# Optimization experiments

Hardware: AMD Instinct MI355X
Metric: run time of the kernel (lower is better)

Reference implementation:

```python
import jax, jax.numpy as jnp
import numpy as np

D = 1024          # n_embd
E = 8             # n_experts
FF = 4 * D        # ffn hidden
CAP = 2048        # expert_capacity
W_IMP = 0.01
W_LOAD = 0.01
LAMBDA_Z = 0.001
W_PEN = 0.01
B, S = 4, 2048
T = B * S


def setup_inputs() -> dict:
    key = jax.random.key(0)
    ks = jax.random.split(key, 8)
    x = jax.random.normal(ks[0], (B, S, D), dtype=jnp.float32)
    gate_w = jax.random.normal(ks[1], (E, D), dtype=jnp.float32) * 0.02   # Linear(D,E) weight
    w1 = jax.random.normal(ks[2], (E, D, FF), dtype=jnp.float32) * 0.02   # c_fc weight per expert
    b1 = jnp.zeros((E, FF), dtype=jnp.float32)
    w2 = jax.random.normal(ks[3], (E, FF, D), dtype=jnp.float32) * 0.02   # c_proj weight per expert
    b2 = jnp.zeros((E, D), dtype=jnp.float32)
    rnd = jax.random.uniform(ks[4], (T,), dtype=jnp.float32)              # torch.rand_like(g2)
    return {"x": x, "gate_w": gate_w, "w1": w1, "b1": b1, "w2": w2, "b2": b2, "rnd": rnd}


def _dispatch_ffn_combine(xf, e_ids, pos, wts, mask, w1, b1, w2, b2):
    """Capacity-buffered dispatch -> grouped FFN -> weighted combine for one routing slot.
    xf: [T,D]; e_ids: [T] int; pos: [T] position within expert; wts: [T] combine weight
    (already zeroed where masked); mask: [T] bool within-capacity (and stochastic) mask."""
    pc = jnp.clip(pos, 0, CAP - 1)
    buf = jnp.zeros((E, CAP, xf.shape[-1]), xf.dtype)
    # masked tokens contribute zeros; valid positions are unique per expert so add == set
    buf = buf.at[e_ids, pc].add(xf * mask[:, None].astype(xf.dtype))
    h = jax.nn.gelu(jnp.einsum('ecd,edf->ecf', buf, w1) + b1[:, None, :], approximate=True)
    out = jnp.einsum('ecf,efd->ecd', h, w2) + b2[:, None, :]          # [E,C,D]
    return out[e_ids, pc] * wts[:, None]                               # [T,D]


def _forward(x, gate_w, w1, b1, w2, b2, rnd):
    xf = x.reshape(-1, x.shape[-1])                                    # [T,D]
    logits = xf @ gate_w.T                                             # [T,E] (bias=False)

    # auxiliary losses
    p166 = jax.nn.softmax(logits / 1.66, axis=-1)
    penalty_a = jnp.mean(p166 * (1.0 - p166))
    pm = p166.mean(axis=0)
    penalty_b = 1.0 / E - jnp.mean(pm * (1.0 - pm))
    penalty = W_PEN * (penalty_a + penalty_b)
    z_loss = LAMBDA_Z * jnp.mean(jax.nn.logsumexp(logits, axis=-1) ** 2)

    probs = jax.nn.softmax(logits.astype(jnp.float32), axis=-1).astype(x.dtype)
    weights, sel = jax.lax.top_k(probs, 2)
    g1, g2 = weights[:, 0], weights[:, 1]
    e1, e2 = sel[:, 0], sel[:, 1]
    denom = g1 + g2
    g1n, g2n = g1 / denom, g2 / denom

    oh1 = jax.nn.one_hot(e1, E, dtype=jnp.int32)
    pos1 = jnp.take_along_axis(jnp.cumsum(oh1, axis=0), e1[:, None], axis=1)[:, 0] - 1
    mask1 = pos1 < CAP
    w_slot1 = g1n * mask1.astype(x.dtype)

    oh2 = jax.nn.one_hot(e2, E, dtype=jnp.int32)
    pos2 = jnp.take_along_axis(jnp.cumsum(oh2, axis=0), e2[:, None], axis=1)[:, 0] - 1
    mask2 = (pos2 < CAP) & (rnd < 2.0 * g2n)
    w_slot2 = g2n * mask2.astype(x.dtype)

    # load-balance loss: f_i from top-1 one-hot, P_i from softmax probs
    f_i = oh1.astype(jnp.float32).mean(axis=0)
    P_i = probs.mean(axis=0)
    load_loss = W_LOAD * E * jnp.sum(f_i * P_i)

    # importance loss over combine matrix G (column sums)
    imp = jnp.zeros((E,), x.dtype).at[e1].add(w_slot1).at[e2].add(w_slot2)
    mean = imp.mean()
    var = jnp.var(imp)
    imp_loss = W_IMP * var / (mean ** 2)

    aux = penalty + z_loss + load_loss + imp_loss

    y = _dispatch_ffn_combine(xf, e1, pos1, w_slot1, mask1, w1, b1, w2, b2)
    y = y + _dispatch_ffn_combine(xf, e2, pos2, w_slot2, mask2, w1, b1, w2, b2)
    return y.reshape(x.shape), aux


def reference(x, gate_w, w1, b1, w2, b2, rnd):
    return _forward(x, gate_w, w1, b1, w2, b2, rnd)
```

## Files before the change

kernel.cpp:

```cpp
#include <hip/hip_runtime.h>
#include <math.h>
#include <stdint.h>

#define DD 1024
#define EE 8
#define FF 4096
#define CAPV 2048
#define TT 8192
#define LIST_STRIDE 4096

typedef __bf16 bf16x8 __attribute__((ext_vector_type(8)));
typedef __bf16 bf16x4 __attribute__((ext_vector_type(4)));
typedef float floatx4 __attribute__((ext_vector_type(4)));
typedef float floatx16 __attribute__((ext_vector_type(16)));

typedef __attribute__((address_space(3))) unsigned int as3_uint;
typedef __attribute__((address_space(1))) const unsigned int as1_uint;

__device__ __forceinline__ void gl_lds16(const void* g, void* l) {
    __builtin_amdgcn_global_load_lds((as1_uint*)g, (as3_uint*)l, 16, 0, 0);
}

__device__ __forceinline__ unsigned short f2bf(float f) {
    union { float f; unsigned int u; } v; v.f = f;
    const unsigned int r = v.u + 0x7FFFu + ((v.u >> 16) & 1u);
    return (unsigned short)(r >> 16);
}

#define GATE_BLOCKS 256
#define T1_BLOCKS 16384
#define T2_BLOCKS 16384

__device__ __forceinline__ void transpose_body(
    const float* __restrict__ in, __bf16* __restrict__ out,
    int K, int N, int bk, int bn, int e, float (*tile)[65], int tid)
{
    const float* ine = in + (size_t)e * K * N;
    __bf16* oute = out + (size_t)e * K * N;
    #pragma unroll
    for (int p = 0; p < 8; ++p) {
        const int idx = p * 256 + tid;
        const int kl = idx >> 5, nl = idx & 31;
        tile[nl][kl] = ine[(size_t)(bk + kl) * N + bn + nl];
    }
    __syncthreads();
    #pragma unroll
    for (int p = 0; p < 4; ++p) {
        const int wdx = p * 256 + tid;
        const int nl = wdx >> 5, c = wdx & 31;
        const unsigned int pk = (unsigned int)f2bf(tile[nl][c * 2])
                              | ((unsigned int)f2bf(tile[nl][c * 2 + 1]) << 16);
        *(unsigned int*)&oute[(size_t)(bn + nl) * K + bk + c * 2] = pk;
    }
}

__global__ __launch_bounds__(256) void moe_prep_kernel(
    const float* __restrict__ x, const float* __restrict__ gw,
    int* __restrict__ e1o, int* __restrict__ e2o,
    float* __restrict__ g1o, float* __restrict__ g2o,
    float* __restrict__ sums, __bf16* __restrict__ xb,
    const float* __restrict__ w1, __bf16* __restrict__ w1T,
    const float* __restrict__ w2, __bf16* __restrict__ w2T)
{
    __shared__ float smem[EE * DD];
    __shared__ float wp[4][26];
    const int bid = blockIdx.x;
    const int tid = threadIdx.x;

    if (bid >= GATE_BLOCKS) {
        float (*tile)[65] = (float (*)[65])smem;
        if (bid < GATE_BLOCKS + T1_BLOCKS) {
            const int f = bid - GATE_BLOCKS;
            transpose_body(w1, w1T, DD, FF, (f & 15) * 64, ((f >> 4) & 127) * 32,
                           f >> 11, tile, tid);
        } else {
            const int f = bid - GATE_BLOCKS - T1_BLOCKS;
            transpose_body(w2, w2T, FF, DD, (f & 63) * 64, ((f >> 6) & 31) * 32,
                           f >> 11, tile, tid);
        }
        return;
    }

    float (*sgw)[DD] = (float (*)[DD])smem;
    for (int i = tid; i < EE * DD; i += 256) sgw[i >> 10][i & 1023] = gw[i];
    __syncthreads();

    const int wave = tid >> 6, lane = tid & 63;
    const int gwave = bid * 4 + wave;
    const int nwaves = GATE_BLOCKS * 4;

    float pa_acc = 0.f, z_acc = 0.f;
    float P_acc[EE] = {0}, p6_acc[EE] = {0};
    int n1_acc[EE] = {0};

    for (int t = gwave; t < TT; t += nwaves) {
        float acc[EE] = {0};
        const float* xr = x + (size_t)t * DD;
        __bf16* xbr = xb + (size_t)t * DD;
        #pragma unroll
        for (int i = 0; i < DD / 64; ++i) {
            const float xv = xr[lane + 64 * i];
            xbr[lane + 64 * i] = (__bf16)xv;
            #pragma unroll
            for (int e = 0; e < EE; ++e) acc[e] += xv * sgw[e][lane + 64 * i];
        }
        #pragma unroll
        for (int e = 0; e < EE; ++e) {
            float v = acc[e];
            #pragma unroll
            for (int off = 32; off > 0; off >>= 1) v += __shfl_xor(v, off, 64);
            acc[e] = v;
        }
        if (lane == 0) {
            float mx = acc[0];
            #pragma unroll
            for (int e = 1; e < EE; ++e) mx = fmaxf(mx, acc[e]);
            float pr[EE], p6[EE], se = 0.f, s6 = 0.f;
            #pragma unroll
            for (int e = 0; e < EE; ++e) {
                pr[e] = __expf(acc[e] - mx); se += pr[e];
                p6[e] = __expf((acc[e] - mx) * (1.0f / 1.66f)); s6 += p6[e];
            }
            const float lse = mx + __logf(se);
            z_acc += lse * lse;
            const float ise = 1.f / se, is6 = 1.f / s6;
            #pragma unroll
            for (int e = 0; e < EE; ++e) {
                pr[e] *= ise; p6[e] *= is6;
                P_acc[e] += pr[e]; p6_acc[e] += p6[e];
                pa_acc += p6[e] * (1.f - p6[e]);
            }
            int a = 0;
            #pragma unroll
            for (int e = 1; e < EE; ++e) if (pr[e] > pr[a]) a = e;
            int b = (a == 0) ? 1 : 0;
            #pragma unroll
            for (int e = 0; e < EE; ++e) if (e != a && pr[e] > pr[b]) b = e;
            n1_acc[a]++;
            const float ga = pr[a], gb = pr[b], idn = 1.f / (ga + gb);
            e1o[t] = a; e2o[t] = b;
            g1o[t] = ga * idn; g2o[t] = gb * idn;
        }
    }
    if (lane == 0) {
        wp[wave][0] = pa_acc; wp[wave][1] = z_acc;
        #pragma unroll
        for (int e = 0; e < EE; ++e) {
            wp[wave][2 + e] = P_acc[e]; wp[wave][10 + e] = p6_acc[e];
            wp[wave][18 + e] = (float)n1_acc[e];
        }
    }
    __syncthreads();
    if (tid < 26) {
        const float s = wp[0][tid] + wp[1][tid] + wp[2][tid] + wp[3][tid];
        atomicAdd(&sums[tid], s);
    }
}

__global__ __launch_bounds__(256) void moe_scan_kernel(
    const int* __restrict__ e1i, const int* __restrict__ e2i,
    const float* __restrict__ g1i, const float* __restrict__ g2i,
    const float* __restrict__ rnd, const float* __restrict__ sums,
    int* __restrict__ etok, int* __restrict__ p1o, int* __restrict__ p2o,
    int* __restrict__ cnt1, int* __restrict__ cnt2,
    float* __restrict__ imp1, float* __restrict__ imp2)
{
    const int bid = blockIdx.x, slot = bid >> 3, e = bid & 7;
    const int tid = threadIdx.x, wave = tid >> 6, lane = tid & 63;
    __shared__ int wtA[4], wtB[4];
    __shared__ float red[256];
    const int* ev = slot ? e2i : e1i;
    const float* gv = slot ? g2i : g1i;
    int* po = slot ? p2o : p1o;
    const int base = slot ? min((int)sums[18 + e], CAPV) : 0;

    int runTot = 0, runM = 0;
    float limp = 0.f;
    for (int c = 0; c < TT / 256; ++c) {
        const int t = c * 256 + tid;
        const int sel = (ev[t] == e) ? 1 : 0;
        const float w = gv[t];
        int ps = sel;
        #pragma unroll
        for (int off = 1; off < 64; off <<= 1) { int v = __shfl_up(ps, off, 64); if (lane >= off) ps += v; }
        if (lane == 63) wtA[wave] = ps;
        __syncthreads();
        int wpre = 0, ctot = 0;
        #pragma unroll
        for (int ww = 0; ww < 4; ++ww) { if (ww < wave) wpre += wtA[ww]; ctot += wtA[ww]; }
        const int pos = runTot + wpre + ps - 1;
        int m, idx;
        if (slot == 0) {
            m = sel && (pos < CAPV);
            idx = pos;
        } else {
            m = (sel && (pos < CAPV) && (rnd[t] < 2.f * w)) ? 1 : 0;
            int pm = m;
            #pragma unroll
            for (int off = 1; off < 64; off <<= 1) { int v = __shfl_up(pm, off, 64); if (lane >= off) pm += v; }
            if (lane == 63) wtB[wave] = pm;
            __syncthreads();
            int wpm = 0, mtot = 0;
            #pragma unroll
            for (int ww = 0; ww < 4; ++ww) { if (ww < wave) wpm += wtB[ww]; mtot += wtB[ww]; }
            idx = runM + wpm + pm - 1;
            runM += mtot;
        }
        if (sel) po[t] = m ? (e * LIST_STRIDE + base + idx) : -1;
        if (m) {
            etok[e * LIST_STRIDE + base + idx] = t;
            limp += w;
        }
        runTot += ctot;
        __syncthreads();
    }
    red[tid] = limp; __syncthreads();
    for (int s = 128; s > 0; s >>= 1) { if (tid < s) red[tid] += red[tid + s]; __syncthreads(); }
    if (tid == 0) {
        if (slot == 0) { cnt1[e] = min(runTot, CAPV); imp1[e] = red[0]; }
        else           { cnt2[e] = runM;              imp2[e] = red[0]; }
    }
}

__global__ void moe_aux_kernel(const float* __restrict__ sums,
                               const float* __restrict__ imp1, const float* __restrict__ imp2,
                               float* __restrict__ out_aux)
{
    if (threadIdx.x != 0 || blockIdx.x != 0) return;
    const float invT = 1.f / (float)TT;
    const float pa = sums[0] / ((float)TT * (float)EE);
    float pb = 0.f, load = 0.f, msum = 0.f;
    float im[EE];
    for (int e = 0; e < EE; ++e) {
        const float pm = sums[10 + e] * invT;
        pb += pm * (1.f - pm);
        load += (sums[18 + e] * invT) * (sums[2 + e] * invT);
        im[e] = imp1[e] + imp2[e];
        msum += im[e];
    }
    pb = 1.f / (float)EE - pb / (float)EE;
    const float penalty = 0.01f * (pa + pb);
    const float z_loss = 0.001f * sums[1] * invT;
    const float load_loss = 0.01f * (float)EE * load;
    const float mean = msum / (float)EE;
    float var = 0.f;
    for (int e = 0; e < EE; ++e) { const float d = im[e] - mean; var += d * d; }
    var /= (float)EE;
    const float imp_loss = 0.01f * var / (mean * mean);
    *out_aux = penalty + z_loss + load_loss + imp_loss;
}

#define FFN_CORE32(NT)                                                         \
    stage(0, 0);                                                               \
    stage(1, 64);                                                              \
    asm volatile("s_waitcnt vmcnt(8)" ::: "memory");                           \
    __builtin_amdgcn_s_barrier();                                              \
    for (int t = 0; t < (NT); ++t) {                                           \
        const int cur = t & 1;                                                 \
        _Pragma("unroll")                                                      \
        for (int ks = 0; ks < 4; ++ks) {                                       \
            bf16x8 av[4], bv[2];                                               \
            const int ch = ((ks * 2 + hi) ^ kx) * 8;                           \
            _Pragma("unroll")                                                  \
            for (int mi = 0; mi < 4; ++mi)                                     \
                av[mi] = *(const bf16x8*)&As[cur][ar[mi] + ch];                 \
            _Pragma("unroll")                                                  \
            for (int nj = 0; nj < 2; ++nj)                                     \
                bv[nj] = *(const bf16x8*)&Bs[cur][br[nj] + ch];                 \
            __builtin_amdgcn_s_setprio(1);                                     \
            _Pragma("unroll")                                                  \
            for (int mi = 0; mi < 4; ++mi)                                     \
                _Pragma("unroll")                                              \
                for (int nj = 0; nj < 2; ++nj)                                 \
                    acc[mi][nj] = __builtin_amdgcn_mfma_f32_32x32x16_bf16(     \
                        bv[nj], av[mi], acc[mi][nj], 0, 0, 0);                 \
            __builtin_amdgcn_s_setprio(0);                                     \
        }                                                                      \
        asm volatile("s_waitcnt lgkmcnt(0)" ::: "memory");                     \
        __builtin_amdgcn_s_barrier();                                          \
        if (t < (NT) - 2) {                                                    \
            stage(cur, (t + 2) * 64);                                          \
            asm volatile("s_waitcnt vmcnt(8)" ::: "memory");                   \
        } else {                                                               \
            asm volatile("s_waitcnt vmcnt(0)" ::: "memory");                   \
        }                                                                      \
        __builtin_amdgcn_s_barrier();                                          \
    }

__global__ __launch_bounds__(512, 2) void moe_ffn1_mfma(
    const __bf16* __restrict__ xb, const __bf16* __restrict__ w1T,
    const float* __restrict__ b1, const int* __restrict__ etok,
    const int* __restrict__ cnt1, const int* __restrict__ cnt2,
    __bf16* __restrict__ H)
{
    const int f = blockIdx.x;
    const int xcd = f & 7, s = f >> 3;
    const int g = xcd * 16 + (s >> 4);
    const int e = g >> 4, n0 = (g & 15) * 256;
    const int m0 = (s & 15) * 256;
    const int ce = cnt1[e] + cnt2[e];
    if (m0 >= ce) return;
    const int tid = threadIdx.x, lane = tid & 63, w = tid >> 6;
    const int wm = w >> 2, wn = w & 3;
    const int l32 = lane & 31, hi = lane >> 5;
    const int kx = l32 & 7;

    __shared__ __bf16 As[2][16384];
    __shared__ __bf16 Bs[2][16384];

    const int srow = tid >> 3;
    const int srcoff = ((tid & 7) ^ (srow & 7)) * 8;
    const __bf16* ap[4];
    const __bf16* bp[4];
    const __bf16* bbase = w1T + (size_t)e * FF * DD;
    #pragma unroll
    for (int r = 0; r < 4; ++r) {
        const int gr = m0 + r * 64 + srow;
        const int tok = (gr < ce) ? etok[e * LIST_STRIDE + gr] : 0;
        ap[r] = xb + (size_t)tok * DD + srcoff;
        bp[r] = bbase + (size_t)(n0 + r * 64 + srow) * DD + srcoff;
    }
    const int ldst = w * 512;

    floatx16 acc[4][2];
    #pragma unroll
    for (int i = 0; i < 4; ++i)
        #pragma unroll
        for (int j = 0; j < 2; ++j)
            #pragma unroll
            for (int q = 0; q < 16; ++q) acc[i][j][q] = 0.f;

    int ar[4], br[2];
    #pragma unroll
    for (int mi = 0; mi < 4; ++mi) ar[mi] = (wm * 128 + mi * 32 + l32) * 64;
    #pragma unroll
    for (int nj = 0; nj < 2; ++nj) br[nj] = (wn * 64 + nj * 32 + l32) * 64;

    auto stage = [&](int bufi, int koff) {
        #pragma unroll
        for (int r = 0; r < 4; ++r)
            gl_lds16(ap[r] + koff, &As[bufi][r * 4096 + ldst]);
        #pragma unroll
        for (int r = 0; r < 4; ++r)
            gl_lds16(bp[r] + koff, &Bs[bufi][r * 4096 + ldst]);
    };

    FFN_CORE32(16)

    const float* b1e = b1 + (size_t)e * FF;
    #pragma unroll
    for (int mi = 0; mi < 4; ++mi) {
        const int mrow = m0 + wm * 128 + mi * 32 + l32;
        __bf16* hrow = H + ((size_t)e * LIST_STRIDE + mrow) * FF;
        #pragma unroll
        for (int nj = 0; nj < 2; ++nj)
            #pragma unroll
            for (int rg = 0; rg < 4; ++rg) {
                const int col0 = n0 + wn * 64 + nj * 32 + rg * 8 + hi * 4;
                const float4 bb = *(const float4*)&b1e[col0];
                float vv[4] = {acc[mi][nj][rg * 4 + 0] + bb.x,
                               acc[mi][nj][rg * 4 + 1] + bb.y,
                               acc[mi][nj][rg * 4 + 2] + bb.z,
                               acc[mi][nj][rg * 4 + 3] + bb.w};
                bf16x4 pk;
                #pragma unroll
                for (int r = 0; r < 4; ++r) {
                    const float v = vv[r];
                    const float u = 0.7978845608028654f * (v + 0.044715f * v * v * v);
                    const float th = 1.f - 2.f / (__expf(2.f * u) + 1.f);
                    pk[r] = (__bf16)(0.5f * v * (1.f + th));
                }
                *(bf16x4*)&hrow[col0] = pk;
            }
    }
}

__global__ __launch_bounds__(512, 2) void moe_ffn2_mfma(
    const __bf16* __restrict__ H, const __bf16* __restrict__ w2T,
    const float* __restrict__ b2, const int* __restrict__ cnt1,
    const int* __restrict__ cnt2, __bf16* __restrict__ O)
{
    const int f = blockIdx.x;
    const int xcd = f & 7, s = f >> 3;
    const int g = xcd * 4 + (s >> 4);
    const int e = g >> 2, n0 = (g & 3) * 256;
    const int m0 = (s & 15) * 256;
    const int ce = cnt1[e] + cnt2[e];
    if (m0 >= ce) return;
    const int tid = threadIdx.x, lane = tid & 63, w = tid >> 6;
    const int wm = w >> 2, wn = w & 3;
    const int l32 = lane & 31, hi = lane >> 5;
    const int kx = l32 & 7;

    __shared__ __bf16 As[2][16384];
    __shared__ __bf16 Bs[2][16384];

    const int srow = tid >> 3;
    const int srcoff = ((tid & 7) ^ (srow & 7)) * 8;
    const __bf16* ap[4];
    const __bf16* bp[4];
    const __bf16* bbase = w2T + (size_t)e * DD * FF;
    #pragma unroll
    for (int r = 0; r < 4; ++r) {
        ap[r] = H + ((size_t)e * LIST_STRIDE + m0 + r * 64 + srow) * FF + srcoff;
        bp[r] = bbase + (size_t)(n0 + r * 64 + srow) * FF + srcoff;
    }
    const int ldst = w * 512;

    floatx16 acc[4][2];
    #pragma unroll
    for (int i = 0; i < 4; ++i)
        #pragma unroll
        for (int j = 0; j < 2; ++j)
            #pragma unroll
            for (int q = 0; q < 16; ++q) acc[i][j][q] = 0.f;

    int ar[4], br[2];
    #pragma unroll
    for (int mi = 0; mi < 4; ++mi) ar[mi] = (wm * 128 + mi * 32 + l32) * 64;
    #pragma unroll
    for (int nj = 0; nj < 2; ++nj) br[nj] = (wn * 64 + nj * 32 + l32) * 64;

    auto stage = [&](int bufi, int koff) {
        #pragma unroll
        for (int r = 0; r < 4; ++r)
            gl_lds16(ap[r] + koff, &As[bufi][r * 4096 + ldst]);
        #pragma unroll
        for (int r = 0; r < 4; ++r)
            gl_lds16(bp[r] + koff, &Bs[bufi][r * 4096 + ldst]);
    };

    FFN_CORE32(64)

    const float* b2e = b2 + (size_t)e * DD;
    #pragma unroll
    for (int mi = 0; mi < 4; ++mi) {
        const int grow = m0 + wm * 128 + mi * 32 + l32;
        if (grow < ce) {
            __bf16* orow = O + ((size_t)e * LIST_STRIDE + grow) * DD;
            #pragma unroll
            for (int nj = 0; nj < 2; ++nj)
                #pragma unroll
                for (int rg = 0; rg < 4; ++rg) {
                    const int col0 = n0 + wn * 64 + nj * 32 + rg * 8 + hi * 4;
                    const float4 bb = *(const float4*)&b2e[col0];
                    bf16x4 pk;
                    pk[0] = (__bf16)(acc[mi][nj][rg * 4 + 0] + bb.x);
                    pk[1] = (__bf16)(acc[mi][nj][rg * 4 + 1] + bb.y);
                    pk[2] = (__bf16)(acc[mi][nj][rg * 4 + 2] + bb.z);
                    pk[3] = (__bf16)(acc[mi][nj][rg * 4 + 3] + bb.w);
                    *(bf16x4*)&orow[col0] = pk;
                }
        }
    }
}

__global__ __launch_bounds__(256) void moe_combine_kernel(
    const __bf16* __restrict__ O, const float* __restrict__ g1v,
    const float* __restrict__ g2v, const int* __restrict__ p1v,
    const int* __restrict__ p2v, float* __restrict__ y)
{
    const int t = blockIdx.x;
    const int col = threadIdx.x * 4;
    const int p1 = p1v[t], p2 = p2v[t];
    float4 r = make_float4(0.f, 0.f, 0.f, 0.f);
    if (p1 >= 0) {
        const float g = g1v[t];
        const bf16x4 v = *(const bf16x4*)&O[(size_t)p1 * DD + col];
        r.x += g * (float)v[0]; r.y += g * (float)v[1];
        r.z += g * (float)v[2]; r.w += g * (float)v[3];
    }
    if (p2 >= 0) {
        const float g = g2v[t];
        const bf16x4 v = *(const bf16x4*)&O[(size_t)p2 * DD + col];
        r.x += g * (float)v[0]; r.y += g * (float)v[1];
        r.z += g * (float)v[2]; r.w += g * (float)v[3];
    }
    *(float4*)&y[(size_t)t * DD + col] = r;
}

extern "C" void kernel_launch(void* const* d_in, const int* in_sizes, int n_in,
                              void* d_out, int out_size, void* d_ws, size_t ws_size,
                              hipStream_t stream) {
    const float* x   = (const float*)d_in[0];
    const float* gw  = (const float*)d_in[1];
    const float* w1  = (const float*)d_in[2];
    const float* b1  = (const float*)d_in[3];
    const float* w2  = (const float*)d_in[4];
    const float* b2  = (const float*)d_in[5];
    const float* rnd = (const float*)d_in[6];
    float* out = (float*)d_out;

    char* p = (char*)d_ws;
    float* sums = (float*)p;
    float* imp1 = (float*)(p + 128);
    float* imp2 = (float*)(p + 160);
    int*   cnt1 = (int*)(p + 192);
    int*   cnt2 = (int*)(p + 224);
    p += 512;
    int*   e1v = (int*)p;   p += TT * 4;
    int*   e2v = (int*)p;   p += TT * 4;
    float* g1v = (float*)p; p += TT * 4;
    float* g2v = (float*)p; p += TT * 4;
    int*   p1v = (int*)p;   p += TT * 4;
    int*   p2v = (int*)p;   p += TT * 4;
    int*   etok = (int*)p;  p += EE * LIST_STRIDE * 4;
    uintptr_t q = (((uintptr_t)p) + 255) & ~(uintptr_t)255;
    __bf16* xb  = (__bf16*)q;  q += (size_t)TT * DD * 2;
    __bf16* w1T = (__bf16*)q;  q += (size_t)EE * FF * DD * 2;
    __bf16* w2T = (__bf16*)q;  q += (size_t)EE * DD * FF * 2;
    __bf16* H   = (__bf16*)q;  q += (size_t)EE * LIST_STRIDE * FF * 2;
    __bf16* O   = (__bf16*)q;

    hipMemsetAsync(sums, 0, 128, stream);

    moe_prep_kernel<<<GATE_BLOCKS + T1_BLOCKS + T2_BLOCKS, 256, 0, stream>>>(
        x, gw, e1v, e2v, g1v, g2v, sums, xb, w1, w1T, w2, w2T);
    moe_scan_kernel<<<16, 256, 0, stream>>>(e1v, e2v, g1v, g2v, rnd, sums,
                                            etok, p1v, p2v, cnt1, cnt2, imp1, imp2);
    moe_aux_kernel<<<1, 64, 0, stream>>>(sums, imp1, imp2, out + (size_t)TT * DD);

    moe_ffn1_mfma<<<2048, 512, 0, stream>>>(xb, w1T, b1, etok, cnt1, cnt2, H);
    moe_ffn2_mfma<<<512, 512, 0, stream>>>(H, w2T, b2, cnt1, cnt2, O);
    moe_combine_kernel<<<TT, 256, 0, stream>>>(O, g1v, g2v, p1v, p2v, out);
}
```

Baseline: 764.9 us.

## Shrink FFN GEMM tiles to 128x128 with 16x16x32 MFMA and 256 threads

```diff
diff --git a/kernel.cpp b/kernel.cpp
--- a/kernel.cpp
+++ b/kernel.cpp
@@ -12,7 +12,6 @@
 typedef __bf16 bf16x8 __attribute__((ext_vector_type(8)));
 typedef __bf16 bf16x4 __attribute__((ext_vector_type(4)));
 typedef float floatx4 __attribute__((ext_vector_type(4)));
-typedef float floatx16 __attribute__((ext_vector_type(16)));
 
 typedef __attribute__((address_space(3))) unsigned int as3_uint;
 typedef __attribute__((address_space(1))) const unsigned int as1_uint;
@@ -250,44 +249,45 @@
     *out_aux = penalty + z_loss + load_loss + imp_loss;
 }
 
-#define FFN_CORE32(NT)                                                         \
+#define FFN_CORE128(NT)                                                        \
     stage(0, 0);                                                               \
-    stage(1, 64);                                                              \
-    asm volatile("s_waitcnt vmcnt(8)" ::: "memory");                           \
+    asm volatile("s_waitcnt vmcnt(0)" ::: "memory");                           \
     __builtin_amdgcn_s_barrier();                                              \
+    _Pragma("unroll 2")                                                        \
     for (int t = 0; t < (NT); ++t) {                                           \
         const int cur = t & 1;                                                 \
+        if (t + 1 < (NT)) stage(cur ^ 1, (t + 1) * 64);                        \
+        bf16x8 a0[4], a1[4], b0[4], b1[4];                                     \
         _Pragma("unroll")                                                      \
-        for (int ks = 0; ks < 4; ++ks) {                                       \
-            bf16x8 av[4], bv[2];                                               \
-            const int ch = ((ks * 2 + hi) ^ kx) * 8;                           \
-            _Pragma("unroll")                                                  \
-            for (int mi = 0; mi < 4; ++mi)                                     \
-                av[mi] = *(const bf16x8*)&As[cur][ar[mi] + ch];                 \
-            _Pragma("unroll")                                                  \
-            for (int nj = 0; nj < 2; ++nj)                                     \
-                bv[nj] = *(const bf16x8*)&Bs[cur][br[nj] + ch];                 \
-            __builtin_amdgcn_s_setprio(1);                                     \
-            _Pragma("unroll")                                                  \
-            for (int mi = 0; mi < 4; ++mi)                                     \
-                _Pragma("unroll")                                              \
-                for (int nj = 0; nj < 2; ++nj)                                 \
-                    acc[mi][nj] = __builtin_amdgcn_mfma_f32_32x32x16_bf16(     \
-                        bv[nj], av[mi], acc[mi][nj], 0, 0, 0);                 \
-            __builtin_amdgcn_s_setprio(0);                                     \
+        for (int i = 0; i < 4; ++i) {                                          \
+            a0[i] = *(const bf16x8*)&As[cur][ar[i] + sw0];                     \
+            a1[i] = *(const bf16x8*)&As[cur][ar[i] + sw1];                     \
+        }                                                                      \
+        _Pragma("unroll")                                                      \
+        for (int j = 0; j < 4; ++j) {                                          \
+            b0[j] = *(const bf16x8*)&Bs[cur][br[j] + sw0];                     \
+            b1[j] = *(const bf16x8*)&Bs[cur][br[j] + sw1];                     \
         }                                                                      \
         asm volatile("s_waitcnt lgkmcnt(0)" ::: "memory");                     \
+        __builtin_amdgcn_s_setprio(1);                                         \
+        _Pragma("unroll")                                                      \
+        for (int i = 0; i < 4; ++i)                                            \
+            _Pragma("unroll")                                                  \
+            for (int j = 0; j < 4; ++j)                                        \
+                acc[i][j] = __builtin_amdgcn_mfma_f32_16x16x32_bf16(           \
+                    b0[j], a0[i], acc[i][j], 0, 0, 0);                         \
+        _Pragma("unroll")                                                      \
+        for (int i = 0; i < 4; ++i)                                            \
+            _Pragma("unroll")                                                  \
+            for (int j = 0; j < 4; ++j)                                        \
+                acc[i][j] = __builtin_amdgcn_mfma_f32_16x16x32_bf16(           \
+                    b1[j], a1[i], acc[i][j], 0, 0, 0);                         \
+        __builtin_amdgcn_s_setprio(0);                                         \
+        asm volatile("s_waitcnt vmcnt(0)" ::: "memory");                       \
         __builtin_amdgcn_s_barrier();                                          \
-        if (t < (NT) - 2) {                                                    \
-            stage(cur, (t + 2) * 64);                                          \
-            asm volatile("s_waitcnt vmcnt(8)" ::: "memory");                   \
-        } else {                                                               \
-            asm volatile("s_waitcnt vmcnt(0)" ::: "memory");                   \
-        }                                                                      \
-        __builtin_amdgcn_s_barrier();                                          \
-    }
-
-__global__ __launch_bounds__(512, 2) void moe_ffn1_mfma(
+    }
+
+__global__ __launch_bounds__(256, 2) void moe_ffn1_mfma(
     const __bf16* __restrict__ xb, const __bf16* __restrict__ w1T,
     const float* __restrict__ b1, const int* __restrict__ etok,
     const int* __restrict__ cnt1, const int* __restrict__ cnt2,
@@ -295,162 +295,154 @@
 {
     const int f = blockIdx.x;
     const int xcd = f & 7, s = f >> 3;
-    const int g = xcd * 16 + (s >> 4);
-    const int e = g >> 4, n0 = (g & 15) * 256;
-    const int m0 = (s & 15) * 256;
+    const int g = xcd * 32 + (s >> 5);
+    const int e = g >> 5, n0 = (g & 31) * 128;
+    const int m0 = (s & 31) * 128;
     const int ce = cnt1[e] + cnt2[e];
     if (m0 >= ce) return;
     const int tid = threadIdx.x, lane = tid & 63, w = tid >> 6;
-    const int wm = w >> 2, wn = w & 3;
-    const int l32 = lane & 31, hi = lane >> 5;
-    const int kx = l32 & 7;
-
-    __shared__ __bf16 As[2][16384];
-    __shared__ __bf16 Bs[2][16384];
-
-    const int srow = tid >> 3;
-    const int srcoff = ((tid & 7) ^ (srow & 7)) * 8;
+    const int wm = w >> 1, wn = w & 1;
+    const int quad = lane >> 4, l16 = lane & 15;
+
+    __shared__ __bf16 As[2][8192];
+    __shared__ __bf16 Bs[2][8192];
+
+    const int srow = tid >> 3, spc = tid & 7;
     const __bf16* ap[4];
     const __bf16* bp[4];
     const __bf16* bbase = w1T + (size_t)e * FF * DD;
     #pragma unroll
-    for (int r = 0; r < 4; ++r) {
-        const int gr = m0 + r * 64 + srow;
+    for (int q = 0; q < 4; ++q) {
+        const int r = q * 32 + srow;
+        const int gr = m0 + r;
         const int tok = (gr < ce) ? etok[e * LIST_STRIDE + gr] : 0;
-        ap[r] = xb + (size_t)tok * DD + srcoff;
-        bp[r] = bbase + (size_t)(n0 + r * 64 + srow) * DD + srcoff;
-    }
-    const int ldst = w * 512;
-
-    floatx16 acc[4][2];
+        const int co = (spc ^ (r & 7)) * 8;
+        ap[q] = xb + (size_t)tok * DD + co;
+        bp[q] = bbase + (size_t)(n0 + r) * DD + co;
+    }
+
+    floatx4 acc[4][4];
     #pragma unroll
     for (int i = 0; i < 4; ++i)
         #pragma unroll
-        for (int j = 0; j < 2; ++j)
-            #pragma unroll
-            for (int q = 0; q < 16; ++q) acc[i][j][q] = 0.f;
-
-    int ar[4], br[2];
-    #pragma unroll
-    for (int mi = 0; mi < 4; ++mi) ar[mi] = (wm * 128 + mi * 32 + l32) * 64;
-    #pragma unroll
-    for (int nj = 0; nj < 2; ++nj) br[nj] = (wn * 64 + nj * 32 + l32) * 64;
+        for (int j = 0; j < 4; ++j) acc[i][j] = floatx4{0.f, 0.f, 0.f, 0.f};
+
+    const int sw0 = (quad ^ (l16 & 7)) * 8;
+    const int sw1 = ((4 + quad) ^ (l16 & 7)) * 8;
+    int ar[4], br[4];
+    #pragma unroll
+    for (int i = 0; i < 4; ++i) ar[i] = (wm * 64 + i * 16 + l16) * 64;
+    #pragma unroll
+    for (int j = 0; j < 4; ++j) br[j] = (wn * 64 + j * 16 + l16) * 64;
 
     auto stage = [&](int bufi, int koff) {
         #pragma unroll
-        for (int r = 0; r < 4; ++r)
-            gl_lds16(ap[r] + koff, &As[bufi][r * 4096 + ldst]);
-        #pragma unroll
-        for (int r = 0; r < 4; ++r)
-            gl_lds16(bp[r] + koff, &Bs[bufi][r * 4096 + ldst]);
+        for (int q = 0; q < 4; ++q)
+            gl_lds16(ap[q] + koff, &As[bufi][q * 2048 + tid * 8]);
+        #pragma unroll
+        for (int q = 0; q < 4; ++q)
+            gl_lds16(bp[q] + koff, &Bs[bufi][q * 2048 + tid * 8]);
     };
 
-    FFN_CORE32(16)
+    FFN_CORE128(16)
 
     const float* b1e = b1 + (size_t)e * FF;
     #pragma unroll
-    for (int mi = 0; mi < 4; ++mi) {
-        const int mrow = m0 + wm * 128 + mi * 32 + l32;
+    for (int i = 0; i < 4; ++i) {
+        const int mrow = m0 + wm * 64 + i * 16 + l16;
         __bf16* hrow = H + ((size_t)e * LIST_STRIDE + mrow) * FF;
         #pragma unroll
-        for (int nj = 0; nj < 2; ++nj)
-            #pragma unroll
-            for (int rg = 0; rg < 4; ++rg) {
-                const int col0 = n0 + wn * 64 + nj * 32 + rg * 8 + hi * 4;
-                const float4 bb = *(const float4*)&b1e[col0];
-                float vv[4] = {acc[mi][nj][rg * 4 + 0] + bb.x,
-                               acc[mi][nj][rg * 4 + 1] + bb.y,
-                               acc[mi][nj][rg * 4 + 2] + bb.z,
-                               acc[mi][nj][rg * 4 + 3] + bb.w};
-                bf16x4 pk;
-                #pragma unroll
-                for (int r = 0; r < 4; ++r) {
-                    const float v = vv[r];
-                    const float u = 0.7978845608028654f * (v + 0.044715f * v * v * v);
-                    const float th = 1.f - 2.f / (__expf(2.f * u) + 1.f);
-                    pk[r] = (__bf16)(0.5f * v * (1.f + th));
-                }
-                *(bf16x4*)&hrow[col0] = pk;
+        for (int j = 0; j < 4; ++j) {
+            const int col0 = n0 + wn * 64 + j * 16 + quad * 4;
+            const float4 bb = *(const float4*)&b1e[col0];
+            float vv[4] = {acc[i][j][0] + bb.x, acc[i][j][1] + bb.y,
+                           acc[i][j][2] + bb.z, acc[i][j][3] + bb.w};
+            bf16x4 pk;
+            #pragma unroll
+            for (int r = 0; r < 4; ++r) {
+                const float v = vv[r];
+                const float u = 0.7978845608028654f * (v + 0.044715f * v * v * v);
+                const float th = 1.f - 2.f / (__expf(2.f * u) + 1.f);
+                pk[r] = (__bf16)(0.5f * v * (1.f + th));
             }
-    }
-}
-
-__global__ __launch_bounds__(512, 2) void moe_ffn2_mfma(
+            *(bf16x4*)&hrow[col0] = pk;
+        }
+    }
+}
+
+__global__ __launch_bounds__(256, 2) void moe_ffn2_mfma(
     const __bf16* __restrict__ H, const __bf16* __restrict__ w2T,
     const float* __restrict__ b2, const int* __restrict__ cnt1,
     const int* __restrict__ cnt2, __bf16* __restrict__ O)
 {
     const int f = blockIdx.x;
     const int xcd = f & 7, s = f >> 3;
-    const int g = xcd * 4 + (s >> 4);
-    const int e = g >> 2, n0 = (g & 3) * 256;
-    const int m0 = (s & 15) * 256;
+    const int g = xcd * 8 + (s >> 5);
+    const int e = g >> 3, n0 = (g & 7) * 128;
+    const int m0 = (s & 31) * 128;
     const int ce = cnt1[e] + cnt2[e];
     if (m0 >= ce) return;
     const int tid = threadIdx.x, lane = tid & 63, w = tid >> 6;
-    const int wm = w >> 2, wn = w & 3;
-    const int l32 = lane & 31, hi = lane >> 5;
-    const int kx = l32 & 7;
-
-    __shared__ __bf16 As[2][16384];
-    __shared__ __bf16 Bs[2][16384];
-
-    const int srow = tid >> 3;
-    const int srcoff = ((tid & 7) ^ (srow & 7)) * 8;
+    const int wm = w >> 1, wn = w & 1;
+    const int quad = lane >> 4, l16 = lane & 15;
+
+    __shared__ __bf16 As[2][8192];
+    __shared__ __bf16 Bs[2][8192];
+
+    const int srow = tid >> 3, spc = tid & 7;
     const __bf16* ap[4];
     const __bf16* bp[4];
     const __bf16* bbase = w2T + (size_t)e * DD * FF;
     #pragma unroll
-    for (int r = 0; r < 4; ++r) {
-        ap[r] = H + ((size_t)e * LIST_STRIDE + m0 + r * 64 + srow) * FF + srcoff;
-        bp[r] = bbase + (size_t)(n0 + r * 64 + srow) * FF + srcoff;
-    }
-    const int ldst = w * 512;
-
-    floatx16 acc[4][2];
+    for (int q = 0; q < 4; ++q) {
+        const int r = q * 32 + srow;
+        const int co = (spc ^ (r & 7)) * 8;
+        ap[q] = H + ((size_t)e * LIST_STRIDE + m0 + r) * FF + co;
+        bp[q] = bbase + (size_t)(n0 + r) * FF + co;
+    }
+
+    floatx4 acc[4][4];
     #pragma unroll
     for (int i = 0; i < 4; ++i)
         #pragma unroll
-        for (int j = 0; j < 2; ++j)
-            #pragma unroll
-            for (int q = 0; q < 16; ++q) acc[i][j][q] = 0.f;
-
-    int ar[4], br[2];
-    #pragma unroll
-    for (int mi = 0; mi < 4; ++mi) ar[mi] = (wm * 128 + mi * 32 + l32) * 64;
-    #pragma unroll
-    for (int nj = 0; nj < 2; ++nj) br[nj] = (wn * 64 + nj * 32 + l32) * 64;
+        for (int j = 0; j < 4; ++j) acc[i][j] = floatx4{0.f, 0.f, 0.f, 0.f};
+
+    const int sw0 = (quad ^ (l16 & 7)) * 8;
+    const int sw1 = ((4 + quad) ^ (l16 & 7)) * 8;
+    int ar[4], br[4];
+    #pragma unroll
+    for (int i = 0; i < 4; ++i) ar[i] = (wm * 64 + i * 16 + l16) * 64;
+    #pragma unroll
+    for (int j = 0; j < 4; ++j) br[j] = (wn * 64 + j * 16 + l16) * 64;
 
     auto stage = [&](int bufi, int koff) {
         #pragma unroll
-        for (int r = 0; r < 4; ++r)
-            gl_lds16(ap[r] + koff, &As[bufi][r * 4096 + ldst]);
-        #pragma unroll
-        for (int r = 0; r < 4; ++r)
-            gl_lds16(bp[r] + koff, &Bs[bufi][r * 4096 + ldst]);
+        for (int q = 0; q < 4; ++q)
+            gl_lds16(ap[q] + koff, &As[bufi][q * 2048 + tid * 8]);
+        #pragma unroll
+        for (int q = 0; q < 4; ++q)
+            gl_lds16(bp[q] + koff, &Bs[bufi][q * 2048 + tid * 8]);
     };
 
-    FFN_CORE32(64)
+    FFN_CORE128(64)
 
     const float* b2e = b2 + (size_t)e * DD;
     #pragma unroll
-    for (int mi = 0; mi < 4; ++mi) {
-        const int grow = m0 + wm * 128 + mi * 32 + l32;
+    for (int i = 0; i < 4; ++i) {
+        const int grow = m0 + wm * 64 + i * 16 + l16;
         if (grow < ce) {
             __bf16* orow = O + ((size_t)e * LIST_STRIDE + grow) * DD;
             #pragma unroll
-            for (int nj = 0; nj < 2; ++nj)
-                #pragma unroll
-                for (int rg = 0; rg < 4; ++rg) {
-                    const int col0 = n0 + wn * 64 + nj * 32 + rg * 8 + hi * 4;
-                    const float4 bb = *(const float4*)&b2e[col0];
-                    bf16x4 pk;
-                    pk[0] = (__bf16)(acc[mi][nj][rg * 4 + 0] + bb.x);
-                    pk[1] = (__bf16)(acc[mi][nj][rg * 4 + 1] + bb.y);
-                    pk[2] = (__bf16)(acc[mi][nj][rg * 4 + 2] + bb.z);
-                    pk[3] = (__bf16)(acc[mi][nj][rg * 4 + 3] + bb.w);
-                    *(bf16x4*)&orow[col0] = pk;
-                }
+            for (int j = 0; j < 4; ++j) {
+                const int col0 = n0 + wn * 64 + j * 16 + quad * 4;
+                const float4 bb = *(const float4*)&b2e[col0];
+                bf16x4 pk;
+                pk[0] = (__bf16)(acc[i][j][0] + bb.x);
+                pk[1] = (__bf16)(acc[i][j][1] + bb.y);
+                pk[2] = (__bf16)(acc[i][j][2] + bb.z);
+                pk[3] = (__bf16)(acc[i][j][3] + bb.w);
+                *(bf16x4*)&orow[col0] = pk;
+            }
         }
     }
 }
@@ -520,7 +512,7 @@
                                             etok, p1v, p2v, cnt1, cnt2, imp1, imp2);
     moe_aux_kernel<<<1, 64, 0, stream>>>(sums, imp1, imp2, out + (size_t)TT * DD);
 
-    moe_ffn1_mfma<<<2048, 512, 0, stream>>>(xb, w1T, b1, etok, cnt1, cnt2, H);
-    moe_ffn2_mfma<<<512, 512, 0, stream>>>(H, w2T, b2, cnt1, cnt2, O);
+    moe_ffn1_mfma<<<8192, 256, 0, stream>>>(xb, w1T, b1, etok, cnt1, cnt2, H);
+    moe_ffn2_mfma<<<2048, 256, 0, stream>>>(H, w2T, b2, cnt1, cnt2, O);
     moe_combine_kernel<<<TT, 256, 0, stream>>>(O, g1v, g2v, p1v, p2v, out);
 }
```

Result: slower. 789.5 us (+3.2%).
